# Kernel optimization log

Measured on AMD Instinct MI355X. Metric: run time of the kernel, lower is better.

## Reference

```python
import jax, jax.numpy as jnp
import numpy as np

N = 4096      # nodes
FIN = 512     # input features
HID = 256     # hidden_features (concat across heads)
H = 4         # n_heads in layer 1
D1 = HID // H # per-head dim layer 1
C = 64        # num_classes
NEG = 0.2     # leaky_relu slope


def setup_inputs() -> dict:
    key = jax.random.key(0)
    ks = jax.random.split(key, 8)
    x = jax.random.normal(ks[0], (N, FIN), jnp.float32)
    A = jax.random.randint(ks[1], (N, N), 0, 2, jnp.int32)
    A = jnp.maximum(A, jnp.eye(N, dtype=jnp.int32))  # self-loops: no all-masked rows
    s = 0.05
    W1 = jax.random.normal(ks[2], (FIN, H * D1), jnp.float32) * s
    a1_src = jax.random.normal(ks[3], (H, D1), jnp.float32) * s
    a1_dst = jax.random.normal(ks[4], (H, D1), jnp.float32) * s
    W2 = jax.random.normal(ks[5], (HID, C), jnp.float32) * s
    a2_src = jax.random.normal(ks[6], (1, C), jnp.float32) * s
    a2_dst = jax.random.normal(ks[7], (1, C), jnp.float32) * s
    return {"x": x, "A": A, "W1": W1, "a1_src": a1_src, "a1_dst": a1_dst,
            "W2": W2, "a2_src": a2_src, "a2_dst": a2_dst}


def gat_layer(x, A, W, a_src, a_dst, is_concat):
    n = x.shape[0]
    h_heads, d = a_src.shape
    h = (x @ W).reshape(n, h_heads, d)                 # [N,H,D]
    s_src = jnp.einsum('nhd,hd->nh', h, a_src)          # [N,H]
    s_dst = jnp.einsum('nhd,hd->nh', h, a_dst)          # [N,H]
    e = s_src[:, None, :] + s_dst[None, :, :]           # [N,N,H]
    e = jnp.where(e >= 0, e, NEG * e)                   # LeakyReLU
    mask = (A > 0)[:, :, None]
    e = jnp.where(mask, e, jnp.float32(-1e9))           # adjacency mask
    alpha = jax.nn.softmax(e, axis=1)                   # softmax over neighbors j
    out = jnp.einsum('ijh,jhd->ihd', alpha, h)          # aggregate
    return out.reshape(n, h_heads * d) if is_concat else out.mean(axis=1)


def reference(x, A, W1, a1_src, a1_dst, W2, a2_src, a2_dst):
    h = gat_layer(x, A, W1, a1_src, a1_dst, True)
    h = jax.nn.elu(h)
    return gat_layer(h, A, W2, a2_src, a2_dst, False)
```

## Files before the change

kernel.cpp:

```cpp
#include <hip/hip_runtime.h>
#include <hip/hip_bf16.h>

#define NN 4096
#define FIN 512
#define HID 256
#define NH 4
#define DD 64
#define NCLS 64

typedef short bf16x8 __attribute__((ext_vector_type(8)));
typedef float f32x4 __attribute__((ext_vector_type(4)));
typedef unsigned int u32x4 __attribute__((ext_vector_type(4)));

__device__ __forceinline__ unsigned fbits(float x) {
    return __builtin_bit_cast(unsigned, x);
}
__device__ __forceinline__ unsigned short f2bf_rne(float x) {
    unsigned u = fbits(x);
    unsigned r = (u + 0x7fffu + ((u >> 16) & 1u)) >> 16;
    return (unsigned short)r;
}

__device__ __forceinline__ bf16x8 pack8(const float* wv) {
    u32x4 au;
#pragma unroll
    for (int t = 0; t < 4; ++t)
        au[t] = __builtin_amdgcn_perm(fbits(wv[2 * t + 1]), fbits(wv[2 * t]),
                                      0x07060302u);
    return __builtin_bit_cast(bf16x8, au);
}

__device__ __forceinline__ bf16x8 ones_frag() {
    u32x4 au = {0x3f803f80u, 0x3f803f80u, 0x3f803f80u, 0x3f803f80u};
    return __builtin_bit_cast(bf16x8, au);
}

__device__ __forceinline__ void compute_probe(int m, int quad, int* pi, int* pn) {
    float xv[8], yv[8];
#pragma unroll
    for (int e = 0; e < 8; ++e) {
        xv[e] = (quad == 0 && e == 0) ? (float)(m + 1) : 0.f;
        yv[e] = (quad == 0 && e == 0) ? 1.f : 0.f;
    }
    bf16x8 x1 = pack8(xv), y1 = pack8(yv);
#pragma unroll
    for (int e = 0; e < 8; ++e) {
        xv[e] = (quad == 0 && e == 0) ? 1.f : 0.f;
        yv[e] = (quad == 0 && e == 0) ? (float)(m + 1) : 0.f;
    }
    bf16x8 x2 = pack8(xv), y2 = pack8(yv);
    f32x4 d1 = {}, d2 = {};
    d1 = __builtin_amdgcn_mfma_f32_16x16x32_bf16(x1, y1, d1, 0, 0, 0);
    d2 = __builtin_amdgcn_mfma_f32_16x16x32_bf16(x2, y2, d2, 0, 0, 0);
#pragma unroll
    for (int r = 0; r < 4; ++r) {
        pi[r] = min(15, max(0, (int)d1[r] - 1));
        pn[r] = min(15, max(0, (int)d2[r] - 1));
    }
}

__global__ __launch_bounds__(256) void adj_bitmask(const int* __restrict__ Adj,
                                                   unsigned* __restrict__ Adjb) {
    const size_t base = (size_t)blockIdx.x * 1024;
    const int tid = threadIdx.x, lane = tid & 63;
#pragma unroll
    for (int c = 0; c < 4; ++c) {
        size_t gid = base + c * 256 + tid;
        int v = Adj[gid];
        unsigned long long bm = __ballot(v > 0);
        if ((lane & 31) == 0)
            Adjb[gid >> 5] = (unsigned)((lane & 32) ? (bm >> 32) : bm);
    }
}

template <int R, int C>
__global__ __launch_bounds__(256) void transpose_cvt(const float* __restrict__ In,
                                                     unsigned short* __restrict__ OutT) {
    __shared__ float t[32][33];
    const int tid = threadIdx.x;
    const int r0 = blockIdx.y * 32, c0 = blockIdx.x * 32;
    const int rl = tid >> 3, cg = tid & 7;
    float4 v = *(const float4*)&In[(size_t)(r0 + rl) * C + c0 + cg * 4];
    t[rl][cg * 4 + 0] = v.x; t[rl][cg * 4 + 1] = v.y;
    t[rl][cg * 4 + 2] = v.z; t[rl][cg * 4 + 3] = v.w;
    __syncthreads();
    const int cl = tid >> 3, rg = tid & 7;
    ushort4 o;
    o.x = f2bf_rne(t[rg * 4 + 0][cl]);
    o.y = f2bf_rne(t[rg * 4 + 1][cl]);
    o.z = f2bf_rne(t[rg * 4 + 2][cl]);
    o.w = f2bf_rne(t[rg * 4 + 3][cl]);
    *(ushort4*)&OutT[(size_t)(c0 + cl) * R + r0 + rg * 4] = o;
}

__device__ __forceinline__ void head_epilogue(
    float (*accx)[16][65], unsigned short (*hbf)[64],
    int tid, int hh, int i0, int n0,
    const float* a_src, const float* a_dst,
    unsigned short* HT, float* ssr, float* EP)
{
    const int row = tid >> 4, cg = tid & 15;
    float ps = 0.f, pd = 0.f;
#pragma unroll
    for (int c4 = 0; c4 < 4; ++c4) {
        int col = cg * 4 + c4;
        float val = accx[0][row][col] + accx[1][row][col] +
                    accx[2][row][col] + accx[3][row][col];
        ps += val * a_src[n0 + col];
        pd += val * a_dst[n0 + col];
        hbf[row][col] = f2bf_rne(val);
    }
#pragma unroll
    for (int o = 8; o >= 1; o >>= 1) {
        ps += __shfl_xor(ps, o, 64);
        pd += __shfl_xor(pd, o, 64);
    }
    if (cg == 0) {
        int node = i0 + row;
        ssr[hh * NN + node] = ps;
        EP[(size_t)(hh * NN + node) * 2 + 0] = __expf(pd);
        EP[(size_t)(hh * NN + node) * 2 + 1] = __expf(0.2f * pd);
    }
    __syncthreads();
    const int c = tid >> 2, rq = tid & 3;
    ushort4 o4;
    o4.x = hbf[rq * 4 + 0][c];
    o4.y = hbf[rq * 4 + 1][c];
    o4.z = hbf[rq * 4 + 2][c];
    o4.w = hbf[rq * 4 + 3][c];
    *(ushort4*)&HT[(size_t)(n0 + c) * NN + i0 + rq * 4] = o4;
}

__global__ __launch_bounds__(256) void gemm_head1(
    const float* __restrict__ x,
    const unsigned short* __restrict__ WT,
    const float* __restrict__ a_src, const float* __restrict__ a_dst,
    unsigned short* __restrict__ HT,
    float* __restrict__ ssr, float* __restrict__ EP)
{
    __shared__ float accx[4][16][65];
    __shared__ unsigned short hbf[16][64];
    const int tid = threadIdx.x;
    const int lane = tid & 63, sp = tid >> 6;
    const int m = lane & 15, quad = lane >> 4;
    const int hh = blockIdx.x, i0 = blockIdx.y * 16;
    const int n0 = hh * 64;
    int pi[4], pn[4];
    compute_probe(m, quad, pi, pn);
    f32x4 acc[4] = {};
#pragma unroll
    for (int ks = 0; ks < 4; ++ks) {
        const int kb = sp * 128 + ks * 32 + quad * 8;
        const float* Af = x + (size_t)(i0 + m) * FIN + kb;
        float4 a0 = *(const float4*)Af;
        float4 a1 = *(const float4*)(Af + 4);
        float av8[8] = {a0.x, a0.y, a0.z, a0.w, a1.x, a1.y, a1.z, a1.w};
        u32x4 au;
#pragma unroll
        for (int t = 0; t < 4; ++t)
            au[t] = (unsigned)f2bf_rne(av8[2 * t]) |
                    ((unsigned)f2bf_rne(av8[2 * t + 1]) << 16);
        bf16x8 a = __builtin_bit_cast(bf16x8, au);
        bf16x8 b[4];
#pragma unroll
        for (int nt = 0; nt < 4; ++nt)
            b[nt] = *(const bf16x8*)&WT[(size_t)(n0 + nt * 16 + m) * FIN + kb];
#pragma unroll
        for (int nt = 0; nt < 4; ++nt)
            acc[nt] = __builtin_amdgcn_mfma_f32_16x16x32_bf16(a, b[nt], acc[nt], 0, 0, 0);
    }
#pragma unroll
    for (int nt = 0; nt < 4; ++nt)
#pragma unroll
        for (int r = 0; r < 4; ++r)
            accx[sp][pi[r]][nt * 16 + pn[r]] = acc[nt][r];
    __syncthreads();
    head_epilogue(accx, hbf, tid, hh, i0, n0, a_src, a_dst, HT, ssr, EP);
}

__global__ __launch_bounds__(256) void gemm_head2(
    const float* __restrict__ numP,
    const float* __restrict__ denP,
    const unsigned short* __restrict__ WT,
    const float* __restrict__ a_src, const float* __restrict__ a_dst,
    unsigned short* __restrict__ HT,
    float* __restrict__ ssr, float* __restrict__ EP)
{
    __shared__ float accx[4][16][65];
    __shared__ unsigned short hbf[16][64];
    const int tid = threadIdx.x;
    const int lane = tid & 63, sp = tid >> 6;
    const int m = lane & 15, quad = lane >> 4;
    const int i0 = blockIdx.x * 16;
    int pi[4], pn[4];
    compute_probe(m, quad, pi, pn);

    const float rd = 1.f / (denP[sp * NN + i0 + m] +
                            denP[NH * NN + sp * NN + i0 + m]);
    f32x4 acc[4] = {};
#pragma unroll
    for (int ks = 0; ks < 2; ++ks) {
        const int kb = sp * 64 + ks * 32 + quad * 8;
        const float* p0 = numP + (size_t)(i0 + m) * HID + kb;
        const float* p1 = p0 + (size_t)NN * HID;
        float4 a0 = *(const float4*)p0;
        float4 a1 = *(const float4*)(p0 + 4);
        float4 b0 = *(const float4*)p1;
        float4 b1 = *(const float4*)(p1 + 4);
        float av8[8] = {a0.x + b0.x, a0.y + b0.y, a0.z + b0.z, a0.w + b0.w,
                        a1.x + b1.x, a1.y + b1.y, a1.z + b1.z, a1.w + b1.w};
        u32x4 au;
#pragma unroll
        for (int t = 0; t < 4; ++t) {
            float v0 = av8[2 * t] * rd;
            float v1 = av8[2 * t + 1] * rd;
            v0 = (v0 > 0.f) ? v0 : (__expf(v0) - 1.f);
            v1 = (v1 > 0.f) ? v1 : (__expf(v1) - 1.f);
            au[t] = (unsigned)f2bf_rne(v0) | ((unsigned)f2bf_rne(v1) << 16);
        }
        bf16x8 a = __builtin_bit_cast(bf16x8, au);
        bf16x8 b[4];
#pragma unroll
        for (int nt = 0; nt < 4; ++nt)
            b[nt] = *(const bf16x8*)&WT[(size_t)(nt * 16 + m) * HID + kb];
#pragma unroll
        for (int nt = 0; nt < 4; ++nt)
            acc[nt] = __builtin_amdgcn_mfma_f32_16x16x32_bf16(a, b[nt], acc[nt], 0, 0, 0);
    }
#pragma unroll
    for (int nt = 0; nt < 4; ++nt)
#pragma unroll
        for (int r = 0; r < 4; ++r)
            accx[sp][pi[r]][nt * 16 + pn[r]] = acc[nt][r];
    __syncthreads();
    head_epilogue(accx, hbf, tid, 0, i0, 0, a_src, a_dst, HT, ssr, EP);
}

template <int IT>
__device__ __forceinline__ void attn_core2(
    const unsigned short* __restrict__ htb,
    const unsigned* __restrict__ Adjb,
    const float* __restrict__ ssh,
    const float* __restrict__ eph,
    const int i0, const int jbase, const int m, const int quad,
    f32x4 (&acc)[IT][4], f32x4 (&accd)[IT])
{
    const bf16x8 ones = ones_frag();
    float E1i[IT], E2i[IT];
    u32x4 mw[IT][2];
#pragma unroll
    for (int t = 0; t < IT; ++t) {
        float ss = ssh[i0 + t * 16 + m];
        E1i[t] = __expf(ss);
        E2i[t] = __expf(0.2f * ss);
        const unsigned* mrow = Adjb + (size_t)(i0 + t * 16 + m) * 128 + (jbase >> 5);
        mw[t][0] = *(const u32x4*)mrow;
        mw[t][1] = *(const u32x4*)(mrow + 4);
    }
#pragma unroll
    for (int s = 0; s < 8; ++s) {
        const int kb = jbase + s * 32 + quad * 8;
        const float* e = eph + 2 * kb;
        f32x4 ep[4];
#pragma unroll
        for (int v = 0; v < 4; ++v) ep[v] = *(const f32x4*)(e + 4 * v);
        bf16x8 bf[4];
#pragma unroll
        for (int nt = 0; nt < 4; ++nt)
            bf[nt] = *(const bf16x8*)&htb[(size_t)(nt * 16 + m) * NN + kb];
#pragma unroll
        for (int t = 0; t < IT; ++t) {
            const unsigned mb = (mw[t][s >> 2][s & 3] >> (quad * 8)) & 0xffu;
            float wv[8];
#pragma unroll
            for (int u = 0; u < 8; ++u) {
                float e1 = ep[u >> 1][(2 * u) & 3];
                float e2 = ep[u >> 1][(2 * u + 1) & 3];
                float w = fmaxf(E1i[t] * e1, E2i[t] * e2);
                wv[u] = ((mb >> u) & 1u) ? w : 0.f;
            }
            bf16x8 av = pack8(wv);
            accd[t] = __builtin_amdgcn_mfma_f32_16x16x32_bf16(av, ones, accd[t], 0, 0, 0);
#pragma unroll
            for (int nt = 0; nt < 4; ++nt)
                acc[t][nt] = __builtin_amdgcn_mfma_f32_16x16x32_bf16(
                    av, bf[nt], acc[t][nt], 0, 0, 0);
        }
    }
}

__global__ __launch_bounds__(512, 4) void attn_l1(
    const unsigned short* __restrict__ HT,
    const unsigned* __restrict__ Adjb,
    const float* __restrict__ ssr,
    const float* __restrict__ EP,
    float* __restrict__ numP,
    float* __restrict__ denP)
{
    __shared__ float accx[2][8][16][65];
    __shared__ float lx[2][8][16];
    const int tid = threadIdx.x;
    const int lane = tid & 63, sp = tid >> 6;
    const int m = lane & 15, quad = lane >> 4;
    const int i0 = blockIdx.x * 32, hh = blockIdx.y, half = blockIdx.z;
    int pi[4], pn[4];
    compute_probe(m, quad, pi, pn);

    const unsigned short* htb = HT + (size_t)(hh * 64) * NN;
    const float* eph = EP + (size_t)hh * NN * 2;
    const float* ssh = ssr + hh * NN;
    const int jbase = half * 2048 + sp * 256;

    f32x4 acc[2][4] = {};
    f32x4 accd[2] = {};
    attn_core2<2>(htb, Adjb, ssh, eph, i0, jbase, m, quad, acc, accd);

#pragma unroll
    for (int t = 0; t < 2; ++t) {
#pragma unroll
        for (int nt = 0; nt < 4; ++nt)
#pragma unroll
            for (int r = 0; r < 4; ++r)
                accx[t][sp][pi[r]][nt * 16 + pn[r]] = acc[t][nt][r];
#pragma unroll
        for (int r = 0; r < 4; ++r) lx[t][sp][pi[r]] = accd[t][r];
    }
    __syncthreads();

#pragma unroll
    for (int e = 0; e < 4; ++e) {
        int idx = tid + e * 512;
        int t = idx >> 10, row = (idx >> 6) & 15, col = idx & 63;
        float num = 0.f, den = 0.f;
#pragma unroll
        for (int s = 0; s < 8; ++s) {
            num += accx[t][s][row][col];
            den += lx[t][s][row];
        }
        int node = i0 + t * 16 + row;
        numP[(size_t)half * NN * HID + (size_t)node * HID + hh * 64 + col] = num;
        if (col == 0) denP[(size_t)half * NH * NN + hh * NN + node] = den;
    }
}

__global__ __launch_bounds__(512, 4) void attn_l2(
    const unsigned short* __restrict__ HT,
    const unsigned* __restrict__ Adjb,
    const float* __restrict__ ssr,
    const float* __restrict__ EP,
    float* __restrict__ numP,
    float* __restrict__ denP)
{
    __shared__ float accx[8][16][65];
    __shared__ float lx[8][16];
    const int tid = threadIdx.x;
    const int lane = tid & 63, sp = tid >> 6;
    const int m = lane & 15, quad = lane >> 4;
    const int i0 = blockIdx.x * 16, half = blockIdx.y;
    int pi[4], pn[4];
    compute_probe(m, quad, pi, pn);
    const int jbase = half * 2048 + sp * 256;

    f32x4 acc[1][4] = {};
    f32x4 accd[1] = {};
    attn_core2<1>(HT, Adjb, ssr, EP, i0, jbase, m, quad, acc, accd);

#pragma unroll
    for (int nt = 0; nt < 4; ++nt)
#pragma unroll
        for (int r = 0; r < 4; ++r)
            accx[sp][pi[r]][nt * 16 + pn[r]] = acc[0][nt][r];
#pragma unroll
    for (int r = 0; r < 4; ++r) lx[sp][pi[r]] = accd[0][r];
    __syncthreads();

#pragma unroll
    for (int e = 0; e < 2; ++e) {
        int idx = tid + e * 512;
        int row = idx >> 6, col = idx & 63;
        float num = 0.f, den = 0.f;
#pragma unroll
        for (int s = 0; s < 8; ++s) {
            num += accx[s][row][col];
            den += lx[s][row];
        }
        int node = i0 + row;
        numP[(size_t)half * NN * 64 + (size_t)node * 64 + col] = num;
        if (col == 0) denP[(size_t)half * NN + node] = den;
    }
}

__global__ __launch_bounds__(256) void combine_out(
    const float* __restrict__ numP, const float* __restrict__ denP,
    float* __restrict__ out)
{
    const int gid = blockIdx.x * 256 + threadIdx.x;
    const int base = gid * 4;
    const int node = base >> 6;
    float4 n0 = *(const float4*)&numP[base];
    float4 n1 = *(const float4*)&numP[(size_t)NN * 64 + base];
    float rd = 1.f / (denP[node] + denP[NN + node]);
    float4 o = make_float4((n0.x + n1.x) * rd, (n0.y + n1.y) * rd,
                           (n0.z + n1.z) * rd, (n0.w + n1.w) * rd);
    *(float4*)&out[base] = o;
}

extern "C" void kernel_launch(void* const* d_in, const int* in_sizes, int n_in,
                              void* d_out, int out_size, void* d_ws, size_t ws_size,
                              hipStream_t stream) {
    const float* x      = (const float*)d_in[0];
    const int*   Adj    = (const int*)d_in[1];
    const float* W1     = (const float*)d_in[2];
    const float* a1_src = (const float*)d_in[3];
    const float* a1_dst = (const float*)d_in[4];
    const float* W2     = (const float*)d_in[5];
    const float* a2_src = (const float*)d_in[6];
    const float* a2_dst = (const float*)d_in[7];
    float* out = (float*)d_out;

    float* ws = (float*)d_ws;
    unsigned short* HT1   = (unsigned short*)ws;
    float*          numP1 = ws + 524288;
    float*          denP1 = ws + 2621440;
    unsigned short* HT2   = (unsigned short*)(ws + 2654208);
    unsigned short* WT1   = (unsigned short*)(ws + 2785280);
    unsigned short* WT2   = (unsigned short*)(ws + 2850816);
    unsigned*       Adjb  = (unsigned*)(ws + 2859008);
    float* s1s   = ws + 3383296;
    float* EP1   = ws + 3399680;
    float* s2s   = ws + 3432448;
    float* EP2   = ws + 3436544;
    float* numP2 = ws + 3444736;
    float* denP2 = ws + 3969024;

    adj_bitmask<<<dim3(16384), 256, 0, stream>>>(Adj, Adjb);
    transpose_cvt<FIN, HID><<<dim3(HID / 32, FIN / 32), 256, 0, stream>>>(W1, WT1);
    transpose_cvt<HID, NCLS><<<dim3(NCLS / 32, HID / 32), 256, 0, stream>>>(W2, WT2);

    gemm_head1<<<dim3(NH, NN / 16), 256, 0, stream>>>(
        x, WT1, a1_src, a1_dst, HT1, s1s, EP1);
    attn_l1<<<dim3(NN / 32, NH, 2), 512, 0, stream>>>(
        HT1, Adjb, s1s, EP1, numP1, denP1);

    gemm_head2<<<dim3(NN / 16), 256, 0, stream>>>(
        numP1, denP1, WT2, a2_src, a2_dst, HT2, s2s, EP2);
    attn_l2<<<dim3(NN / 16, 2), 512, 0, stream>>>(
        HT2, Adjb, s2s, EP2, numP2, denP2);
    combine_out<<<dim3(256), 256, 0, stream>>>(numP2, denP2, out);
}
```

Baseline: 206.6 us.

## Share HT tiles across waves via double-buffered LDS in attention kernels

The attention kernels now have each wave own a different 32-row block of query nodes while the four waves cooperatively load one shared HT/EP slice into a double-buffered LDS tile. Before, each wave read its own j-range directly from global memory. The j dimension is split into more partitions (4 for layer 1, 16 for layer 2), and the partial sums are reduced in gemm_head2 and combine_out. This is meant to cut redundant global loads of HT and raise data reuse. In exchange it adds a __syncthreads per step, more partial-sum traffic in the workspace, and a larger reduction in the downstream kernels.

```diff
diff --git a/kernel.cpp b/kernel.cpp
--- a/kernel.cpp
+++ b/kernel.cpp
@@ -195,20 +195,25 @@
     int pi[4], pn[4];
     compute_probe(m, quad, pi, pn);
 
-    const float rd = 1.f / (denP[sp * NN + i0 + m] +
-                            denP[NH * NN + sp * NN + i0 + m]);
+    float den = 0.f;
+#pragma unroll
+    for (int q = 0; q < 4; ++q)
+        den += denP[((size_t)q * NH + sp) * NN + i0 + m];
+    const float rd = 1.f / den;
+
     f32x4 acc[4] = {};
 #pragma unroll
     for (int ks = 0; ks < 2; ++ks) {
         const int kb = sp * 64 + ks * 32 + quad * 8;
-        const float* p0 = numP + (size_t)(i0 + m) * HID + kb;
-        const float* p1 = p0 + (size_t)NN * HID;
-        float4 a0 = *(const float4*)p0;
-        float4 a1 = *(const float4*)(p0 + 4);
-        float4 b0 = *(const float4*)p1;
-        float4 b1 = *(const float4*)(p1 + 4);
-        float av8[8] = {a0.x + b0.x, a0.y + b0.y, a0.z + b0.z, a0.w + b0.w,
-                        a1.x + b1.x, a1.y + b1.y, a1.z + b1.z, a1.w + b1.w};
+        float av8[8] = {};
+#pragma unroll
+        for (int q = 0; q < 4; ++q) {
+            const float* pq = numP + ((size_t)q * NN + (i0 + m)) * HID + kb;
+            float4 a0 = *(const float4*)pq;
+            float4 a1 = *(const float4*)(pq + 4);
+            av8[0] += a0.x; av8[1] += a0.y; av8[2] += a0.z; av8[3] += a0.w;
+            av8[4] += a1.x; av8[5] += a1.y; av8[6] += a1.z; av8[7] += a1.w;
+        }
         u32x4 au;
 #pragma unroll
         for (int t = 0; t < 4; ++t) {
@@ -236,60 +241,86 @@
     head_epilogue(accx, hbf, tid, 0, i0, 0, a_src, a_dst, HT, ssr, EP);
 }
 
-template <int IT>
-__device__ __forceinline__ void attn_core2(
+template <int IT, int NSTEP>
+__device__ __forceinline__ void attn_lds_core(
     const unsigned short* __restrict__ htb,
     const unsigned* __restrict__ Adjb,
     const float* __restrict__ ssh,
     const float* __restrict__ eph,
-    const int i0, const int jbase, const int m, const int quad,
+    const int wave_i0, const int jbase,
+    const int w, const int lane, const int m, const int quad,
+    bf16x8 (*HTb)[256], f32x4 (*EPb)[16],
     f32x4 (&acc)[IT][4], f32x4 (&accd)[IT])
 {
+    constexpr int NG = NSTEP / 4;
     const bf16x8 ones = ones_frag();
     float E1i[IT], E2i[IT];
-    u32x4 mw[IT][2];
+    const unsigned* mrow[IT];
+    u32x4 mcur[IT], mnext[IT];
 #pragma unroll
     for (int t = 0; t < IT; ++t) {
-        float ss = ssh[i0 + t * 16 + m];
+        float ss = ssh[wave_i0 + t * 16 + m];
         E1i[t] = __expf(ss);
         E2i[t] = __expf(0.2f * ss);
-        const unsigned* mrow = Adjb + (size_t)(i0 + t * 16 + m) * 128 + (jbase >> 5);
-        mw[t][0] = *(const u32x4*)mrow;
-        mw[t][1] = *(const u32x4*)(mrow + 4);
-    }
-#pragma unroll
-    for (int s = 0; s < 8; ++s) {
-        const int kb = jbase + s * 32 + quad * 8;
-        const float* e = eph + 2 * kb;
-        f32x4 ep[4];
-#pragma unroll
-        for (int v = 0; v < 4; ++v) ep[v] = *(const f32x4*)(e + 4 * v);
-        bf16x8 bf[4];
-#pragma unroll
-        for (int nt = 0; nt < 4; ++nt)
-            bf[nt] = *(const bf16x8*)&htb[(size_t)(nt * 16 + m) * NN + kb];
-#pragma unroll
-        for (int t = 0; t < IT; ++t) {
-            const unsigned mb = (mw[t][s >> 2][s & 3] >> (quad * 8)) & 0xffu;
-            float wv[8];
-#pragma unroll
-            for (int u = 0; u < 8; ++u) {
-                float e1 = ep[u >> 1][(2 * u) & 3];
-                float e2 = ep[u >> 1][(2 * u + 1) & 3];
-                float w = fmaxf(E1i[t] * e1, E2i[t] * e2);
-                wv[u] = ((mb >> u) & 1u) ? w : 0.f;
+        mrow[t] = Adjb + (size_t)(wave_i0 + t * 16 + m) * 128 + (jbase >> 5);
+        mcur[t] = *(const u32x4*)mrow[t];
+    }
+    const size_t hrow = (size_t)(w * 16 + m) * NN;
+    bf16x8 htv = *(const bf16x8*)&htb[hrow + jbase + quad * 8];
+    const bool epl = (w == 0 && lane < 16);
+    f32x4 epv = {};
+    if (epl) epv = *(const f32x4*)(eph + 2 * jbase + lane * 4);
+
+    for (int g = 0; g < NG; ++g) {
+        if (g + 1 < NG) {
+#pragma unroll
+            for (int t = 0; t < IT; ++t)
+                mnext[t] = *(const u32x4*)(mrow[t] + g * 4 + 4);
+        }
+#pragma unroll
+        for (int si = 0; si < 4; ++si) {
+            const int s = g * 4 + si;
+            const int buf = si & 1;
+            HTb[buf][w * 64 + lane] = htv;
+            if (epl) EPb[buf][lane] = epv;
+            __syncthreads();
+            if (s + 1 < NSTEP) {
+                const int kb2 = jbase + (s + 1) * 32;
+                htv = *(const bf16x8*)&htb[hrow + kb2 + quad * 8];
+                if (epl) epv = *(const f32x4*)(eph + 2 * kb2 + lane * 4);
             }
-            bf16x8 av = pack8(wv);
-            accd[t] = __builtin_amdgcn_mfma_f32_16x16x32_bf16(av, ones, accd[t], 0, 0, 0);
-#pragma unroll
-            for (int nt = 0; nt < 4; ++nt)
-                acc[t][nt] = __builtin_amdgcn_mfma_f32_16x16x32_bf16(
-                    av, bf[nt], acc[t][nt], 0, 0, 0);
-        }
-    }
-}
-
-__global__ __launch_bounds__(512, 4) void attn_l1(
+            f32x4 ep[4];
+            bf16x8 bfr[4];
+#pragma unroll
+            for (int v = 0; v < 4; ++v) ep[v] = EPb[buf][quad * 4 + v];
+#pragma unroll
+            for (int nt = 0; nt < 4; ++nt) bfr[nt] = HTb[buf][nt * 64 + lane];
+#pragma unroll
+            for (int t = 0; t < IT; ++t) {
+                const unsigned mb = (mcur[t][si] >> (quad * 8)) & 0xffu;
+                float wv[8];
+#pragma unroll
+                for (int u = 0; u < 8; ++u) {
+                    float e1 = ep[u >> 1][(2 * u) & 3];
+                    float e2 = ep[u >> 1][(2 * u + 1) & 3];
+                    float wgt = fmaxf(E1i[t] * e1, E2i[t] * e2);
+                    wv[u] = ((mb >> u) & 1u) ? wgt : 0.f;
+                }
+                bf16x8 av = pack8(wv);
+                accd[t] = __builtin_amdgcn_mfma_f32_16x16x32_bf16(av, ones, accd[t], 0, 0, 0);
+#pragma unroll
+                for (int nt = 0; nt < 4; ++nt)
+                    acc[t][nt] = __builtin_amdgcn_mfma_f32_16x16x32_bf16(
+                        av, bfr[nt], acc[t][nt], 0, 0, 0);
+            }
+        }
+#pragma unroll
+        for (int t = 0; t < IT; ++t) mcur[t] = mnext[t];
+    }
+    __syncthreads();
+}
+
+__global__ __launch_bounds__(256, 2) void attn_l1(
     const unsigned short* __restrict__ HT,
     const unsigned* __restrict__ Adjb,
     const float* __restrict__ ssr,
@@ -297,53 +328,50 @@
     float* __restrict__ numP,
     float* __restrict__ denP)
 {
-    __shared__ float accx[2][8][16][65];
-    __shared__ float lx[2][8][16];
+    __shared__ bf16x8 HTb[2][256];
+    __shared__ f32x4 EPb[2][16];
+    __shared__ __align__(16) float accx[4][16][68];
+    __shared__ float lx[4][16];
     const int tid = threadIdx.x;
-    const int lane = tid & 63, sp = tid >> 6;
+    const int lane = tid & 63, w = tid >> 6;
     const int m = lane & 15, quad = lane >> 4;
-    const int i0 = blockIdx.x * 32, hh = blockIdx.y, half = blockIdx.z;
+    const int i0 = blockIdx.x * 128, hh = blockIdx.y, qtr = blockIdx.z;
     int pi[4], pn[4];
     compute_probe(m, quad, pi, pn);
 
     const unsigned short* htb = HT + (size_t)(hh * 64) * NN;
     const float* eph = EP + (size_t)hh * NN * 2;
     const float* ssh = ssr + hh * NN;
-    const int jbase = half * 2048 + sp * 256;
 
     f32x4 acc[2][4] = {};
     f32x4 accd[2] = {};
-    attn_core2<2>(htb, Adjb, ssh, eph, i0, jbase, m, quad, acc, accd);
-
+    attn_lds_core<2, 32>(htb, Adjb, ssh, eph, i0 + w * 32, qtr * 1024,
+                         w, lane, m, quad, HTb, EPb, acc, accd);
+
+    const int orow = tid >> 4, ocol = (tid & 15) * 4;
 #pragma unroll
     for (int t = 0; t < 2; ++t) {
 #pragma unroll
         for (int nt = 0; nt < 4; ++nt)
 #pragma unroll
             for (int r = 0; r < 4; ++r)
-                accx[t][sp][pi[r]][nt * 16 + pn[r]] = acc[t][nt][r];
-#pragma unroll
-        for (int r = 0; r < 4; ++r) lx[t][sp][pi[r]] = accd[t][r];
-    }
-    __syncthreads();
-
-#pragma unroll
-    for (int e = 0; e < 4; ++e) {
-        int idx = tid + e * 512;
-        int t = idx >> 10, row = (idx >> 6) & 15, col = idx & 63;
-        float num = 0.f, den = 0.f;
-#pragma unroll
-        for (int s = 0; s < 8; ++s) {
-            num += accx[t][s][row][col];
-            den += lx[t][s][row];
-        }
-        int node = i0 + t * 16 + row;
-        numP[(size_t)half * NN * HID + (size_t)node * HID + hh * 64 + col] = num;
-        if (col == 0) denP[(size_t)half * NH * NN + hh * NN + node] = den;
-    }
-}
-
-__global__ __launch_bounds__(512, 4) void attn_l2(
+                accx[w][pi[r]][nt * 16 + pn[r]] = acc[t][nt][r];
+#pragma unroll
+        for (int r = 0; r < 4; ++r) lx[w][pi[r]] = accd[t][r];
+        __syncthreads();
+#pragma unroll
+        for (int p = 0; p < 4; ++p) {
+            int node = i0 + p * 32 + t * 16 + orow;
+            f32x4 v = *(const f32x4*)&accx[p][orow][ocol];
+            *(f32x4*)&numP[((size_t)qtr * NN + node) * HID + hh * 64 + ocol] = v;
+            if (ocol == 0)
+                denP[((size_t)qtr * NH + hh) * NN + node] = lx[p][orow];
+        }
+        __syncthreads();
+    }
+}
+
+__global__ __launch_bounds__(256, 2) void attn_l2(
     const unsigned short* __restrict__ HT,
     const unsigned* __restrict__ Adjb,
     const float* __restrict__ ssr,
@@ -351,42 +379,41 @@
     float* __restrict__ numP,
     float* __restrict__ denP)
 {
-    __shared__ float accx[8][16][65];
-    __shared__ float lx[8][16];
+    __shared__ bf16x8 HTb[2][256];
+    __shared__ f32x4 EPb[2][16];
+    __shared__ __align__(16) float accx[4][16][68];
+    __shared__ float lx[4][16];
     const int tid = threadIdx.x;
-    const int lane = tid & 63, sp = tid >> 6;
+    const int lane = tid & 63, w = tid >> 6;
     const int m = lane & 15, quad = lane >> 4;
-    const int i0 = blockIdx.x * 16, half = blockIdx.y;
+    const int i0 = blockIdx.x * 128, jsp = blockIdx.y;
     int pi[4], pn[4];
     compute_probe(m, quad, pi, pn);
-    const int jbase = half * 2048 + sp * 256;
-
-    f32x4 acc[1][4] = {};
-    f32x4 accd[1] = {};
-    attn_core2<1>(HT, Adjb, ssr, EP, i0, jbase, m, quad, acc, accd);
-
-#pragma unroll
-    for (int nt = 0; nt < 4; ++nt)
-#pragma unroll
-        for (int r = 0; r < 4; ++r)
-            accx[sp][pi[r]][nt * 16 + pn[r]] = acc[0][nt][r];
-#pragma unroll
-    for (int r = 0; r < 4; ++r) lx[sp][pi[r]] = accd[0][r];
-    __syncthreads();
-
-#pragma unroll
-    for (int e = 0; e < 2; ++e) {
-        int idx = tid + e * 512;
-        int row = idx >> 6, col = idx & 63;
-        float num = 0.f, den = 0.f;
-#pragma unroll
-        for (int s = 0; s < 8; ++s) {
-            num += accx[s][row][col];
-            den += lx[s][row];
-        }
-        int node = i0 + row;
-        numP[(size_t)half * NN * 64 + (size_t)node * 64 + col] = num;
-        if (col == 0) denP[(size_t)half * NN + node] = den;
+
+    f32x4 acc[2][4] = {};
+    f32x4 accd[2] = {};
+    attn_lds_core<2, 8>(HT, Adjb, ssr, EP, i0 + w * 32, jsp * 256,
+                        w, lane, m, quad, HTb, EPb, acc, accd);
+
+    const int orow = tid >> 4, ocol = (tid & 15) * 4;
+#pragma unroll
+    for (int t = 0; t < 2; ++t) {
+#pragma unroll
+        for (int nt = 0; nt < 4; ++nt)
+#pragma unroll
+            for (int r = 0; r < 4; ++r)
+                accx[w][pi[r]][nt * 16 + pn[r]] = acc[t][nt][r];
+#pragma unroll
+        for (int r = 0; r < 4; ++r) lx[w][pi[r]] = accd[t][r];
+        __syncthreads();
+#pragma unroll
+        for (int p = 0; p < 4; ++p) {
+            int node = i0 + p * 32 + t * 16 + orow;
+            f32x4 v = *(const f32x4*)&accx[p][orow][ocol];
+            *(f32x4*)&numP[((size_t)jsp * NN + node) * 64 + ocol] = v;
+            if (ocol == 0) denP[(size_t)jsp * NN + node] = lx[p][orow];
+        }
+        __syncthreads();
     }
 }
 
@@ -396,12 +423,16 @@
 {
     const int gid = blockIdx.x * 256 + threadIdx.x;
     const int base = gid * 4;
-    const int node = base >> 6;
-    float4 n0 = *(const float4*)&numP[base];
-    float4 n1 = *(const float4*)&numP[(size_t)NN * 64 + base];
-    float rd = 1.f / (denP[node] + denP[NN + node]);
-    float4 o = make_float4((n0.x + n1.x) * rd, (n0.y + n1.y) * rd,
-                           (n0.z + n1.z) * rd, (n0.w + n1.w) * rd);
+    const int node = base >> 6, col = base & 63;
+    float nx = 0.f, ny = 0.f, nz = 0.f, nw = 0.f, den = 0.f;
+#pragma unroll
+    for (int p = 0; p < 16; ++p) {
+        float4 v = *(const float4*)&numP[((size_t)p * NN + node) * 64 + col];
+        nx += v.x; ny += v.y; nz += v.z; nw += v.w;
+        den += denP[(size_t)p * NN + node];
+    }
+    float rd = 1.f / den;
+    float4 o = make_float4(nx * rd, ny * rd, nz * rd, nw * rd);
     *(float4*)&out[base] = o;
 }
 
@@ -421,17 +452,17 @@
     float* ws = (float*)d_ws;
     unsigned short* HT1   = (unsigned short*)ws;
     float*          numP1 = ws + 524288;
-    float*          denP1 = ws + 2621440;
-    unsigned short* HT2   = (unsigned short*)(ws + 2654208);
-    unsigned short* WT1   = (unsigned short*)(ws + 2785280);
-    unsigned short* WT2   = (unsigned short*)(ws + 2850816);
-    unsigned*       Adjb  = (unsigned*)(ws + 2859008);
-    float* s1s   = ws + 3383296;
-    float* EP1   = ws + 3399680;
-    float* s2s   = ws + 3432448;
-    float* EP2   = ws + 3436544;
-    float* numP2 = ws + 3444736;
-    float* denP2 = ws + 3969024;
+    float*          denP1 = ws + 4718592;
+    unsigned short* HT2   = (unsigned short*)(ws + 4784128);
+    unsigned short* WT1   = (unsigned short*)(ws + 4915200);
+    unsigned short* WT2   = (unsigned short*)(ws + 4980736);
+    unsigned*       Adjb  = (unsigned*)(ws + 4988928);
+    float* s1s   = ws + 5513216;
+    float* EP1   = ws + 5529600;
+    float* s2s   = ws + 5562368;
+    float* EP2   = ws + 5566464;
+    float* numP2 = ws + 5574656;
+    float* denP2 = ws + 9768960;
 
     adj_bitmask<<<dim3(16384), 256, 0, stream>>>(Adj, Adjb);
     transpose_cvt<FIN, HID><<<dim3(HID / 32, FIN / 32), 256, 0, stream>>>(W1, WT1);
@@ -439,12 +470,12 @@
 
     gemm_head1<<<dim3(NH, NN / 16), 256, 0, stream>>>(
         x, WT1, a1_src, a1_dst, HT1, s1s, EP1);
-    attn_l1<<<dim3(NN / 32, NH, 2), 512, 0, stream>>>(
+    attn_l1<<<dim3(NN / 128, NH, 4), 256, 0, stream>>>(
         HT1, Adjb, s1s, EP1, numP1, denP1);
 
     gemm_head2<<<dim3(NN / 16), 256, 0, stream>>>(
         numP1, denP1, WT2, a2_src, a2_dst, HT2, s2s, EP2);
-    attn_l2<<<dim3(NN / 16, 2), 512, 0, stream>>>(
+    attn_l2<<<dim3(NN / 128, 16), 256, 0, stream>>>(
         HT2, Adjb, s2s, EP2, numP2, denP2);
     combine_out<<<dim3(256), 256, 0, stream>>>(numP2, denP2, out);
 }
```

Result: faster. 176.7 us (-14.5%).
